# Kernel optimization log

Measured on AMD Instinct MI355X. Metric: run time of the kernel, lower is better.

The kernel has to match this reference:

```python
import jax, jax.numpy as jnp
import numpy as np

B, T, D = 2, 2048, 1024
H = 16
DH = D // H


def setup_inputs() -> dict:
    key = jax.random.key(0)
    ks = jax.random.split(key, 6)
    s = 1.0 / np.sqrt(D)
    return {
        "input_emb": jax.random.normal(ks[0], (B, T, D), dtype=jnp.float32),
        "W_key": jax.random.normal(ks[1], (D, D), dtype=jnp.float32) * s,
        "W_query": jax.random.normal(ks[2], (D, D), dtype=jnp.float32) * s,
        "W_value": jax.random.normal(ks[3], (D, D), dtype=jnp.float32) * s,
        "W_out": jax.random.normal(ks[4], (D, D), dtype=jnp.float32) * s,
        "b_out": jnp.zeros((D,), dtype=jnp.float32),
    }


def reference(input_emb, W_key, W_query, W_value, W_out, b_out):
    b, t, _ = input_emb.shape
    # projections (no bias on K/Q/V, matching bias_on=False)
    k = (input_emb @ W_key).reshape(b, t, H, DH).transpose(0, 2, 1, 3)    # [b,h,t,dh]
    q = (input_emb @ W_query).reshape(b, t, H, DH).transpose(0, 2, 1, 3)
    v = (input_emb @ W_value).reshape(b, t, H, DH).transpose(0, 2, 1, 3)
    # NOTE: source computes K @ Q^T (not Q @ K^T) — reproduce faithfully.
    scores = jnp.einsum("bhid,bhjd->bhij", k, q) / jnp.sqrt(jnp.float32(DH))
    mask = jnp.triu(jnp.ones((t, t), dtype=bool), k=1)                    # True where j > i
    scores = jnp.where(mask, -jnp.inf, scores)
    attn = jax.nn.softmax(scores, axis=-1)                                # softmax over j (query axis)
    ctx = jnp.einsum("bhij,bhjd->bhid", attn, v)                          # [b,h,t,dh]
    ctx = ctx.transpose(0, 2, 1, 3).reshape(b, t, H * DH)                 # [b,t,d]
    return ctx @ W_out + b_out
```

## Files before the change

kernel.cpp:

```cpp
#include <hip/hip_runtime.h>
#include <cstdint>
#include <cstddef>

#define T_SEQ 2048
#define DMODEL 1024
#define NHEAD 16
#define DHEAD 64
#define BATCH 2
#define MROWS (BATCH * T_SEQ)

typedef __attribute__((ext_vector_type(8))) short bf16x8;
typedef __attribute__((ext_vector_type(4))) float f32x4;
typedef unsigned int u32;

__device__ __forceinline__ unsigned short f2bf(float f) {
  u32 u = __float_as_uint(f);
  u32 r = (u + 0x7FFFu + ((u >> 16) & 1u)) >> 16;
  return (unsigned short)r;
}

__device__ __forceinline__ u32 cvtpk(float a, float b) {
  u32 r;
  asm("v_cvt_pk_bf16_f32 %0, %1, %2" : "=v"(r) : "v"(a), "v"(b));
  return r;
}

__device__ __forceinline__ void gl_lds16(const unsigned short* g, unsigned short* l) {
  __builtin_amdgcn_global_load_lds(
      (const __attribute__((address_space(1))) u32*)g,
      (__attribute__((address_space(3))) u32*)l, 16, 0, 0);
}

__global__ void k_prep(const float* __restrict__ X, unsigned short* __restrict__ Xb,
                       const float* __restrict__ W0, const float* __restrict__ W1,
                       const float* __restrict__ W2, const float* __restrict__ W3,
                       unsigned short* __restrict__ T0, unsigned short* __restrict__ T1,
                       unsigned short* __restrict__ T2, unsigned short* __restrict__ T3) {
  const int bid = blockIdx.x;
  if (bid < 4096) {
    int i = (bid * 256 + threadIdx.x) * 4;
    float4 v = *reinterpret_cast<const float4*>(X + i);
    ushort4 o;
    o.x = f2bf(v.x); o.y = f2bf(v.y); o.z = f2bf(v.z); o.w = f2bf(v.w);
    *reinterpret_cast<ushort4*>(Xb + i) = o;
    return;
  }
  const int b2 = bid - 4096;
  const int z = b2 >> 10;
  const int rem = b2 & 1023;
  const int cx = rem & 31, ry = rem >> 5;
  const float* W = (z == 0) ? W0 : (z == 1) ? W1 : (z == 2) ? W2 : W3;
  unsigned short* Wt = (z == 0) ? T0 : (z == 1) ? T1 : (z == 2) ? T2 : T3;
  __shared__ float tile[32][33];
  const int c0 = cx * 32, r0 = ry * 32;
  const int tx = threadIdx.x & 31, ty = threadIdx.x >> 5;
#pragma unroll
  for (int i = ty; i < 32; i += 8)
    tile[i][tx] = W[(size_t)(r0 + i) * DMODEL + c0 + tx];
  __syncthreads();
#pragma unroll
  for (int i = ty; i < 32; i += 8)
    Wt[(size_t)(c0 + i) * DMODEL + r0 + tx] = f2bf(tile[tx][i]);
}

__global__ __launch_bounds__(256, 2)
void k_gemm_qkv(const unsigned short* __restrict__ Xb,
                const unsigned short* __restrict__ Wkt,
                const unsigned short* __restrict__ Wqt,
                const unsigned short* __restrict__ Wvt,
                unsigned short* __restrict__ Qr,
                unsigned short* __restrict__ Kr,
                unsigned short* __restrict__ Vt)
{
  __shared__ __align__(16) unsigned short As[128 * 32];
  __shared__ __align__(16) unsigned short Bs[128 * 32];
  const int orig = blockIdx.x;
  const int t = (orig & 7) * 96 + (orig >> 3);
  const int z = t >> 8;
  const int remt = t & 255;
  const int by = remt >> 3, bx = remt & 7;
  const unsigned short* Bt = (z == 0) ? Wkt : (z == 1) ? Wqt : Wvt;

  const int tid = threadIdx.x;
  const int lane = tid & 63, w = tid >> 6;
  const int wr = w >> 1, wc = w & 1;
  const int l15 = lane & 15, l4 = lane >> 4;
  const int m0 = by * 128, n0 = bx * 128;

  f32x4 acc[4][4] = {};

  for (int k0 = 0; k0 < DMODEL; k0 += 32) {
#pragma unroll
    for (int i = 0; i < 2; ++i) {
      int c = i * 256 + tid;
      int row = c >> 2, cc = c & 3;
      gl_lds16(Xb + (size_t)(m0 + row) * DMODEL + k0 + cc * 8, As + c * 8);
      gl_lds16(Bt + (size_t)(n0 + row) * DMODEL + k0 + cc * 8, Bs + c * 8);
    }
    __syncthreads();
    bf16x8 af[4], bfr[4];
#pragma unroll
    for (int mi = 0; mi < 4; ++mi)
      af[mi] = *reinterpret_cast<const bf16x8*>(As + (wr * 64 + mi * 16 + l15) * 32 + l4 * 8);
#pragma unroll
    for (int ni = 0; ni < 4; ++ni)
      bfr[ni] = *reinterpret_cast<const bf16x8*>(Bs + (wc * 64 + ni * 16 + l15) * 32 + l4 * 8);
#pragma unroll
    for (int mi = 0; mi < 4; ++mi)
#pragma unroll
      for (int ni = 0; ni < 4; ++ni)
        acc[mi][ni] = __builtin_amdgcn_mfma_f32_16x16x32_bf16(af[mi], bfr[ni], acc[mi][ni], 0, 0, 0);
    __syncthreads();
  }

  if (z < 2) {
    unsigned short* C = (z == 0) ? Qr : Kr;
#pragma unroll
    for (int mi = 0; mi < 4; ++mi)
#pragma unroll
      for (int ni = 0; ni < 4; ++ni) {
        const int col = n0 + wc * 64 + ni * 16 + l15;
        const int rowb = m0 + wr * 64 + mi * 16 + l4 * 4;
#pragma unroll
        for (int r = 0; r < 4; ++r)
          C[(size_t)(rowb + r) * DMODEL + col] = f2bf(acc[mi][ni][r]);
      }
  } else {
#pragma unroll
    for (int mi = 0; mi < 4; ++mi)
#pragma unroll
      for (int ni = 0; ni < 4; ++ni) {
        const int col = n0 + wc * 64 + ni * 16 + l15;
        const int h = col >> 6, dh = col & 63;
        const int rowb = m0 + wr * 64 + mi * 16 + l4 * 4;
        const int b = rowb >> 11, tt = rowb & (T_SEQ - 1);
        const int tl = tt & 63;
        const int tp = (tt & ~63) | (tl & 32) | ((tl & 12) << 1) | ((tl & 16) >> 2);
        unsigned short* p = Vt + ((size_t)(b * NHEAD + h) * DHEAD + dh) * T_SEQ + tp;
        ushort4 pkv;
        pkv.x = f2bf(acc[mi][ni][0]); pkv.y = f2bf(acc[mi][ni][1]);
        pkv.z = f2bf(acc[mi][ni][2]); pkv.w = f2bf(acc[mi][ni][3]);
        *reinterpret_cast<ushort4*>(p) = pkv;
      }
  }
}

__global__ __launch_bounds__(256, 2)
void k_attn(const unsigned short* __restrict__ Qr,
            const unsigned short* __restrict__ Kr,
            const unsigned short* __restrict__ Vp,
            unsigned short* __restrict__ ctx)
{
  __shared__ __align__(16) char lds[65536];
  const int tid = threadIdx.x;
  const int lane = tid & 63, w = tid >> 6;
  const int l15 = lane & 15, l4 = lane >> 4;

  const int x = blockIdx.x;
  const int xcd = x & 7, idx = x >> 3;
  const int bh = xcd + 8 * (idx & 3);
  const int cpair = idx >> 2;
  const int b = bh >> 4, h = bh & 15;

  const unsigned short* Qbase = Qr + (size_t)b * T_SEQ * DMODEL + h * DHEAD;
  const unsigned short* Kbase = Kr + (size_t)b * T_SEQ * DMODEL + h * DHEAD;
  const unsigned short* Vbase = Vp + (size_t)bh * DHEAD * T_SEQ;
  unsigned short* obase = ctx + (size_t)b * T_SEQ * DMODEL + h * DHEAD;

  const float SC = 0.18033688011112042f;
  const float M0 = 12.0f;
  const int srow = tid >> 3, scb = tid & 7;
  const int scolE = (scb ^ (srow & 7)) << 3;

  const int sw = (l15 & 7) << 4;
  const char* aK0 = lds + l15 * 128 + ((l4 * 16) ^ sw);
  const char* aK1 = lds + l15 * 128 + (((64 + l4 * 16)) ^ sw);

  const unsigned short* kp = Kbase + (size_t)srow * DMODEL + scolE;
  const unsigned short* vpb = Vbase + (size_t)srow * T_SEQ + scolE;

#define KRD(P, st, ni, v1) (*reinterpret_cast<const bf16x8*>(((v1) ? aK1 : aK0) + (P) * 16384 + (st) * 8192 + (ni) * 2048))
#define VRD(P, st, df, hk) (*reinterpret_cast<const bf16x8*>(((hk) ? aK1 : aK0) + 32768 + (P) * 16384 + (st) * 8192 + (df) * 2048))

#define STAGE(KD, VD, kg, vg)                                                     \
      {                                                                           \
        gl_lds16((kg), (KD) + tid * 8);                                           \
        gl_lds16((kg) + 32 * DMODEL, (KD) + 2048 + tid * 8);                      \
        gl_lds16((kg) + 64 * DMODEL, (KD) + 4096 + tid * 8);                      \
        gl_lds16((kg) + 96 * DMODEL, (KD) + 6144 + tid * 8);                      \
        gl_lds16((vg), (VD) + tid * 8);                                           \
        gl_lds16((vg) + 32 * T_SEQ, (VD) + 2048 + tid * 8);                       \
        gl_lds16((vg) + 64, (VD) + 4096 + tid * 8);                               \
        gl_lds16((vg) + 32 * T_SEQ + 64, (VD) + 6144 + tid * 8);                  \
      }

#define GROUP_BODY(g, P)                                                          \
    {                                                                             \
      const int kv0 = (g) * 128;                                                  \
      const bool diag = ((g) == NG - 1);                                          \
      __builtin_amdgcn_sched_barrier(0);                                          \
      asm volatile("s_waitcnt vmcnt(0)" ::: "memory");                            \
      __builtin_amdgcn_sched_barrier(0);                                          \
      __builtin_amdgcn_s_barrier();                                               \
      __builtin_amdgcn_sched_barrier(0);                                          \
      if ((g) + 1 < NG) {                                                         \
        unsigned short* Kn = (unsigned short*)(lds + ((P) ^ 1) * 16384);          \
        unsigned short* Vn = (unsigned short*)(lds + 32768 + ((P) ^ 1) * 16384);  \
        STAGE(Kn, Vn, kstage, vstage)                                             \
        kstage += 128 * DMODEL; vstage += 128;                                    \
      }                                                                           \
      __builtin_amdgcn_sched_barrier(0);                                          \
      const bool a1 = !diag || codd;                                              \
      const int nlim0 = (diag && !codd) ? (w + 1) : 4;                            \
      const int nlim1 = (diag && codd) ? (w + 1) : 4;                             \
      f32x4 S[2][4] = {};                                                         \
      __builtin_amdgcn_s_setprio(1);                                              \
      _Pragma("unroll")                                                           \
      for (int ni = 0; ni < 4; ++ni)                                              \
        if (ni < nlim0) {                                                         \
          S[0][ni] = __builtin_amdgcn_mfma_f32_16x16x32_bf16(KRD(P, 0, ni, 0), qf[0], S[0][ni], 0, 0, 0); \
          S[0][ni] = __builtin_amdgcn_mfma_f32_16x16x32_bf16(KRD(P, 0, ni, 1), qf[1], S[0][ni], 0, 0, 0); \
        }                                                                         \
      if (a1) {                                                                   \
        _Pragma("unroll")                                                         \
        for (int ni = 0; ni < 4; ++ni)                                            \
          if (ni < nlim1) {                                                       \
            S[1][ni] = __builtin_amdgcn_mfma_f32_16x16x32_bf16(KRD(P, 1, ni, 0), qf[0], S[1][ni], 0, 0, 0); \
            S[1][ni] = __builtin_amdgcn_mfma_f32_16x16x32_bf16(KRD(P, 1, ni, 1), qf[1], S[1][ni], 0, 0, 0); \
          }                                                                       \
      }                                                                           \
      __builtin_amdgcn_s_setprio(0);                                              \
      if (diag) {                                                                 \
        if (!codd) {                                                              \
          _Pragma("unroll")                                                       \
          for (int ni = 0; ni < 4; ++ni)                                          \
            if (ni < nlim0) {                                                     \
              _Pragma("unroll")                                                   \
              for (int r = 0; r < 4; ++r)                                         \
                if (kv0 + ni * 16 + l4 * 4 + r > qrow) S[0][ni][r] = -INFINITY;   \
            }                                                                     \
        } else {                                                                  \
          _Pragma("unroll")                                                       \
          for (int ni = 0; ni < 4; ++ni)                                          \
            if (ni < nlim1) {                                                     \
              _Pragma("unroll")                                                   \
              for (int r = 0; r < 4; ++r)                                         \
                if (kv0 + 64 + ni * 16 + l4 * 4 + r > qrow) S[1][ni][r] = -INFINITY; \
            }                                                                     \
        }                                                                         \
      }                                                                           \
      union __align__(16) PW { u32 u[2][2][4]; bf16x8 v[2][2]; } pw = {};         \
      _Pragma("unroll")                                                           \
      for (int ni = 0; ni < 4; ++ni)                                              \
        if (ni < nlim0) {                                                         \
          const float p0 = __builtin_amdgcn_exp2f(__builtin_fmaf(S[0][ni][0], SC, -M0)); \
          const float p1 = __builtin_amdgcn_exp2f(__builtin_fmaf(S[0][ni][1], SC, -M0)); \
          const float p2 = __builtin_amdgcn_exp2f(__builtin_fmaf(S[0][ni][2], SC, -M0)); \
          const float p3 = __builtin_amdgcn_exp2f(__builtin_fmaf(S[0][ni][3], SC, -M0)); \
          lP += (p0 + p1) + (p2 + p3);                                            \
          pw.u[0][ni >> 1][(ni & 1) * 2]     = cvtpk(p0, p1);                     \
          pw.u[0][ni >> 1][(ni & 1) * 2 + 1] = cvtpk(p2, p3);                     \
        }                                                                         \
      if (a1) {                                                                   \
        _Pragma("unroll")                                                         \
        for (int ni = 0; ni < 4; ++ni)                                            \
          if (ni < nlim1) {                                                       \
            const float p0 = __builtin_amdgcn_exp2f(__builtin_fmaf(S[1][ni][0], SC, -M0)); \
            const float p1 = __builtin_amdgcn_exp2f(__builtin_fmaf(S[1][ni][1], SC, -M0)); \
            const float p2 = __builtin_amdgcn_exp2f(__builtin_fmaf(S[1][ni][2], SC, -M0)); \
            const float p3 = __builtin_amdgcn_exp2f(__builtin_fmaf(S[1][ni][3], SC, -M0)); \
            lP += (p0 + p1) + (p2 + p3);                                          \
            pw.u[1][ni >> 1][(ni & 1) * 2]     = cvtpk(p0, p1);                   \
            pw.u[1][ni >> 1][(ni & 1) * 2 + 1] = cvtpk(p2, p3);                   \
          }                                                                       \
      }                                                                           \
      __builtin_amdgcn_s_setprio(1);                                              \
      {                                                                           \
        const int hkl0 = (diag && !codd) ? ((nlim0 + 1) >> 1) : 2;                \
        _Pragma("unroll")                                                         \
        for (int hk = 0; hk < 2; ++hk)                                            \
          if (hk < hkl0) {                                                        \
            _Pragma("unroll")                                                     \
            for (int df = 0; df < 4; ++df)                                        \
              O[df] = __builtin_amdgcn_mfma_f32_16x16x32_bf16(VRD(P, 0, df, hk), pw.v[0][hk], O[df], 0, 0, 0); \
          }                                                                       \
      }                                                                           \
      if (a1) {                                                                   \
        const int hkl1 = (diag && codd) ? ((nlim1 + 1) >> 1) : 2;                 \
        _Pragma("unroll")                                                         \
        for (int hk = 0; hk < 2; ++hk)                                            \
          if (hk < hkl1) {                                                        \
            _Pragma("unroll")                                                     \
            for (int df = 0; df < 4; ++df)                                        \
              O[df] = __builtin_amdgcn_mfma_f32_16x16x32_bf16(VRD(P, 1, df, hk), pw.v[1][hk], O[df], 0, 0, 0); \
          }                                                                       \
      }                                                                           \
      __builtin_amdgcn_s_setprio(0);                                              \
      __builtin_amdgcn_sched_barrier(0);                                          \
    }

  for (int half = 0; half < 2; ++half) {
    const int c = half ? (31 - cpair) : cpair;
    const bool codd = (c & 1) != 0;
    const int q0w = c * 64 + w * 16;
    const int NG = (c + 2) >> 1;
    const int qrow = q0w + l15;

    bf16x8 qf[2];
#pragma unroll
    for (int ks = 0; ks < 2; ++ks)
      qf[ks] = *reinterpret_cast<const bf16x8*>(
          Qbase + (size_t)(q0w + l15) * DMODEL + ks * 32 + l4 * 8);

    __builtin_amdgcn_sched_barrier(0);
    __builtin_amdgcn_s_barrier();
    __builtin_amdgcn_sched_barrier(0);
    {
      unsigned short* Ks = (unsigned short*)(lds);
      unsigned short* Vs = (unsigned short*)(lds + 32768);
      STAGE(Ks, Vs, kp, vpb)
    }
    const unsigned short* kstage = kp + 128 * DMODEL;
    const unsigned short* vstage = vpb + 128;

    f32x4 O[4] = {};
    float lP = 0.f;

    for (int g2 = 0; g2 < NG; g2 += 2) {
      GROUP_BODY(g2, 0)
      if (g2 + 1 < NG) GROUP_BODY(g2 + 1, 1)
    }

    float lS = lP;
    lS += __shfl_xor(lS, 16);
    lS += __shfl_xor(lS, 32);
    const float rinv = 1.0f / lS;
#pragma unroll
    for (int df = 0; df < 4; ++df) {
      ushort4 o;
      o.x = f2bf(O[df][0] * rinv);
      o.y = f2bf(O[df][1] * rinv);
      o.z = f2bf(O[df][2] * rinv);
      o.w = f2bf(O[df][3] * rinv);
      *reinterpret_cast<ushort4*>(obase + (size_t)qrow * DMODEL + df * 16 + l4 * 4) = o;
    }
  }
#undef GROUP_BODY
#undef STAGE
#undef KRD
#undef VRD
}

__global__ __launch_bounds__(256, 2)
void k_gemm_out(const unsigned short* __restrict__ Ab,
                const unsigned short* __restrict__ Bt,
                const float* __restrict__ bias,
                float* __restrict__ C)
{
  __shared__ __align__(16) unsigned short As[128 * 32];
  __shared__ __align__(16) unsigned short Bs[128 * 32];
  const int orig = blockIdx.x;
  const int t = (orig & 7) * 32 + (orig >> 3);
  const int by = t >> 3, bx = t & 7;

  const int tid = threadIdx.x;
  const int lane = tid & 63, w = tid >> 6;
  const int wr = w >> 1, wc = w & 1;
  const int l15 = lane & 15, l4 = lane >> 4;
  const int m0 = by * 128, n0 = bx * 128;

  f32x4 acc[4][4] = {};

  for (int k0 = 0; k0 < DMODEL; k0 += 32) {
#pragma unroll
    for (int i = 0; i < 2; ++i) {
      int c = i * 256 + tid;
      int row = c >> 2, cc = c & 3;
      gl_lds16(Ab + (size_t)(m0 + row) * DMODEL + k0 + cc * 8, As + c * 8);
      gl_lds16(Bt + (size_t)(n0 + row) * DMODEL + k0 + cc * 8, Bs + c * 8);
    }
    __syncthreads();
    bf16x8 af[4], bfr[4];
#pragma unroll
    for (int mi = 0; mi < 4; ++mi)
      af[mi] = *reinterpret_cast<const bf16x8*>(As + (wr * 64 + mi * 16 + l15) * 32 + l4 * 8);
#pragma unroll
    for (int ni = 0; ni < 4; ++ni)
      bfr[ni] = *reinterpret_cast<const bf16x8*>(Bs + (wc * 64 + ni * 16 + l15) * 32 + l4 * 8);
#pragma unroll
    for (int mi = 0; mi < 4; ++mi)
#pragma unroll
      for (int ni = 0; ni < 4; ++ni)
        acc[mi][ni] = __builtin_amdgcn_mfma_f32_16x16x32_bf16(af[mi], bfr[ni], acc[mi][ni], 0, 0, 0);
    __syncthreads();
  }

#pragma unroll
  for (int mi = 0; mi < 4; ++mi)
#pragma unroll
    for (int ni = 0; ni < 4; ++ni) {
      const int col = n0 + wc * 64 + ni * 16 + l15;
      const float bv = bias[col];
      const int rowb = m0 + wr * 64 + mi * 16 + l4 * 4;
#pragma unroll
      for (int r = 0; r < 4; ++r)
        C[(size_t)(rowb + r) * DMODEL + col] = acc[mi][ni][r] + bv;
    }
}

extern "C" void kernel_launch(void* const* d_in, const int* in_sizes, int n_in,
                              void* d_out, int out_size, void* d_ws, size_t ws_size,
                              hipStream_t stream) {
  const float* X  = (const float*)d_in[0];
  const float* Wk = (const float*)d_in[1];
  const float* Wq = (const float*)d_in[2];
  const float* Wv = (const float*)d_in[3];
  const float* Wo = (const float*)d_in[4];
  const float* bo = (const float*)d_in[5];
  float* out = (float*)d_out;

  char* ws = (char*)d_ws;
  const size_t MB = 1024 * 1024;
  unsigned short* Xb  = (unsigned short*)(ws + 0 * MB);
  unsigned short* Wkt = (unsigned short*)(ws + 8 * MB);
  unsigned short* Wqt = (unsigned short*)(ws + 10 * MB);
  unsigned short* Wvt = (unsigned short*)(ws + 12 * MB);
  unsigned short* Wot = (unsigned short*)(ws + 14 * MB);
  unsigned short* Qr  = (unsigned short*)(ws + 16 * MB);
  unsigned short* Kr  = (unsigned short*)(ws + 24 * MB);
  unsigned short* Vt  = (unsigned short*)(ws + 32 * MB);
  unsigned short* Ctx = (unsigned short*)(ws + 40 * MB);

  k_prep<<<8192, 256, 0, stream>>>(X, Xb, Wk, Wq, Wv, Wo, Wkt, Wqt, Wvt, Wot);
  k_gemm_qkv<<<768, 256, 0, stream>>>(Xb, Wkt, Wqt, Wvt, Qr, Kr, Vt);
  k_attn<<<dim3(512), 256, 0, stream>>>(Qr, Kr, Vt, Ctx);
  k_gemm_out<<<256, 256, 0, stream>>>(Ctx, Wot, bo, out);
}
```

Measured before the change: 103.5 us.

## Double-buffer LDS tiles in QKV and output GEMMs to overlap loads with MFMA

Both projection GEMMs now use two LDS buffers per operand and prefetch the next K-slice via direct global-to-LDS loads while MFMAs run on the current slice. This replaces the load-sync-compute-sync loop with a single barrier per step. Staging addresses are precomputed, and the MFMA block is bracketed with s_setprio to favour matrix issue. LDS use per block doubles, which may limit occupancy, and the manual waitcnt and sched_barrier sequencing constrains the compiler's scheduling.

Measured after the change: 102.7 us. No clear change (-0.8%).

```diff
diff --git a/kernel.cpp b/kernel.cpp
--- a/kernel.cpp
+++ b/kernel.cpp
@@ -72,8 +72,8 @@
                 unsigned short* __restrict__ Kr,
                 unsigned short* __restrict__ Vt)
 {
-  __shared__ __align__(16) unsigned short As[128 * 32];
-  __shared__ __align__(16) unsigned short Bs[128 * 32];
+  __shared__ __align__(16) unsigned short As[2][128 * 32];
+  __shared__ __align__(16) unsigned short Bs[2][128 * 32];
   const int orig = blockIdx.x;
   const int t = (orig & 7) * 96 + (orig >> 3);
   const int z = t >> 8;
@@ -87,31 +87,59 @@
   const int l15 = lane & 15, l4 = lane >> 4;
   const int m0 = by * 128, n0 = bx * 128;
 
+  const int srow = tid >> 2, scc = tid & 3;
+  const unsigned short* Ab0 = Xb + (size_t)(m0 + srow) * DMODEL + scc * 8;
+  const unsigned short* Bb0 = Bt + (size_t)(n0 + srow) * DMODEL + scc * 8;
+  const unsigned short* Ab1 = Ab0 + (size_t)64 * DMODEL;
+  const unsigned short* Bb1 = Bb0 + (size_t)64 * DMODEL;
+
+#define GSTAGE(buf, k0)                                                   \
+  {                                                                       \
+    gl_lds16(Ab0 + (k0), As[buf] + tid * 8);                              \
+    gl_lds16(Ab1 + (k0), As[buf] + 2048 + tid * 8);                       \
+    gl_lds16(Bb0 + (k0), Bs[buf] + tid * 8);                              \
+    gl_lds16(Bb1 + (k0), Bs[buf] + 2048 + tid * 8);                       \
+  }
+
+#define GCOMP(buf)                                                        \
+  {                                                                       \
+    bf16x8 af[4], bfr[4];                                                 \
+    _Pragma("unroll")                                                     \
+    for (int mi = 0; mi < 4; ++mi)                                        \
+      af[mi] = *reinterpret_cast<const bf16x8*>(As[buf] + (wr * 64 + mi * 16 + l15) * 32 + l4 * 8); \
+    _Pragma("unroll")                                                     \
+    for (int ni = 0; ni < 4; ++ni)                                        \
+      bfr[ni] = *reinterpret_cast<const bf16x8*>(Bs[buf] + (wc * 64 + ni * 16 + l15) * 32 + l4 * 8); \
+    __builtin_amdgcn_s_setprio(1);                                        \
+    _Pragma("unroll")                                                     \
+    for (int mi = 0; mi < 4; ++mi)                                        \
+      _Pragma("unroll")                                                   \
+      for (int ni = 0; ni < 4; ++ni)                                      \
+        acc[mi][ni] = __builtin_amdgcn_mfma_f32_16x16x32_bf16(af[mi], bfr[ni], acc[mi][ni], 0, 0, 0); \
+    __builtin_amdgcn_s_setprio(0);                                        \
+  }
+
+#define GSYNC                                                             \
+  __builtin_amdgcn_sched_barrier(0);                                      \
+  asm volatile("s_waitcnt vmcnt(0)" ::: "memory");                        \
+  __builtin_amdgcn_s_barrier();                                           \
+  __builtin_amdgcn_sched_barrier(0);
+
   f32x4 acc[4][4] = {};
 
-  for (int k0 = 0; k0 < DMODEL; k0 += 32) {
-#pragma unroll
-    for (int i = 0; i < 2; ++i) {
-      int c = i * 256 + tid;
-      int row = c >> 2, cc = c & 3;
-      gl_lds16(Xb + (size_t)(m0 + row) * DMODEL + k0 + cc * 8, As + c * 8);
-      gl_lds16(Bt + (size_t)(n0 + row) * DMODEL + k0 + cc * 8, Bs + c * 8);
-    }
-    __syncthreads();
-    bf16x8 af[4], bfr[4];
-#pragma unroll
-    for (int mi = 0; mi < 4; ++mi)
-      af[mi] = *reinterpret_cast<const bf16x8*>(As + (wr * 64 + mi * 16 + l15) * 32 + l4 * 8);
-#pragma unroll
-    for (int ni = 0; ni < 4; ++ni)
-      bfr[ni] = *reinterpret_cast<const bf16x8*>(Bs + (wc * 64 + ni * 16 + l15) * 32 + l4 * 8);
-#pragma unroll
-    for (int mi = 0; mi < 4; ++mi)
-#pragma unroll
-      for (int ni = 0; ni < 4; ++ni)
-        acc[mi][ni] = __builtin_amdgcn_mfma_f32_16x16x32_bf16(af[mi], bfr[ni], acc[mi][ni], 0, 0, 0);
-    __syncthreads();
-  }
+  GSTAGE(0, 0)
+  GSYNC
+  for (int k0 = 0; k0 < DMODEL; k0 += 64) {
+    GSTAGE(1, k0 + 32)
+    GCOMP(0)
+    GSYNC
+    if (k0 + 64 < DMODEL) { GSTAGE(0, k0 + 64) }
+    GCOMP(1)
+    GSYNC
+  }
+#undef GSTAGE
+#undef GCOMP
+#undef GSYNC
 
   if (z < 2) {
     unsigned short* C = (z == 0) ? Qr : Kr;
@@ -357,8 +385,8 @@
                 const float* __restrict__ bias,
                 float* __restrict__ C)
 {
-  __shared__ __align__(16) unsigned short As[128 * 32];
-  __shared__ __align__(16) unsigned short Bs[128 * 32];
+  __shared__ __align__(16) unsigned short As[2][128 * 32];
+  __shared__ __align__(16) unsigned short Bs[2][128 * 32];
   const int orig = blockIdx.x;
   const int t = (orig & 7) * 32 + (orig >> 3);
   const int by = t >> 3, bx = t & 7;
@@ -369,31 +397,59 @@
   const int l15 = lane & 15, l4 = lane >> 4;
   const int m0 = by * 128, n0 = bx * 128;
 
+  const int srow = tid >> 2, scc = tid & 3;
+  const unsigned short* Ab0 = Ab + (size_t)(m0 + srow) * DMODEL + scc * 8;
+  const unsigned short* Bb0 = Bt + (size_t)(n0 + srow) * DMODEL + scc * 8;
+  const unsigned short* Ab1 = Ab0 + (size_t)64 * DMODEL;
+  const unsigned short* Bb1 = Bb0 + (size_t)64 * DMODEL;
+
+#define GSTAGE(buf, k0)                                                   \
+  {                                                                       \
+    gl_lds16(Ab0 + (k0), As[buf] + tid * 8);                              \
+    gl_lds16(Ab1 + (k0), As[buf] + 2048 + tid * 8);                       \
+    gl_lds16(Bb0 + (k0), Bs[buf] + tid * 8);                              \
+    gl_lds16(Bb1 + (k0), Bs[buf] + 2048 + tid * 8);                       \
+  }
+
+#define GCOMP(buf)                                                        \
+  {                                                                       \
+    bf16x8 af[4], bfr[4];                                                 \
+    _Pragma("unroll")                                                     \
+    for (int mi = 0; mi < 4; ++mi)                                        \
+      af[mi] = *reinterpret_cast<const bf16x8*>(As[buf] + (wr * 64 + mi * 16 + l15) * 32 + l4 * 8); \
+    _Pragma("unroll")                                                     \
+    for (int ni = 0; ni < 4; ++ni)                                        \
+      bfr[ni] = *reinterpret_cast<const bf16x8*>(Bs[buf] + (wc * 64 + ni * 16 + l15) * 32 + l4 * 8); \
+    __builtin_amdgcn_s_setprio(1);                                        \
+    _Pragma("unroll")                                                     \
+    for (int mi = 0; mi < 4; ++mi)                                        \
+      _Pragma("unroll")                                                   \
+      for (int ni = 0; ni < 4; ++ni)                                      \
+        acc[mi][ni] = __builtin_amdgcn_mfma_f32_16x16x32_bf16(af[mi], bfr[ni], acc[mi][ni], 0, 0, 0); \
+    __builtin_amdgcn_s_setprio(0);                                        \
+  }
+
+#define GSYNC                                                             \
+  __builtin_amdgcn_sched_barrier(0);                                      \
+  asm volatile("s_waitcnt vmcnt(0)" ::: "memory");                        \
+  __builtin_amdgcn_s_barrier();                                           \
+  __builtin_amdgcn_sched_barrier(0);
+
   f32x4 acc[4][4] = {};
 
-  for (int k0 = 0; k0 < DMODEL; k0 += 32) {
-#pragma unroll
-    for (int i = 0; i < 2; ++i) {
-      int c = i * 256 + tid;
-      int row = c >> 2, cc = c & 3;
-      gl_lds16(Ab + (size_t)(m0 + row) * DMODEL + k0 + cc * 8, As + c * 8);
-      gl_lds16(Bt + (size_t)(n0 + row) * DMODEL + k0 + cc * 8, Bs + c * 8);
-    }
-    __syncthreads();
-    bf16x8 af[4], bfr[4];
-#pragma unroll
-    for (int mi = 0; mi < 4; ++mi)
-      af[mi] = *reinterpret_cast<const bf16x8*>(As + (wr * 64 + mi * 16 + l15) * 32 + l4 * 8);
-#pragma unroll
-    for (int ni = 0; ni < 4; ++ni)
-      bfr[ni] = *reinterpret_cast<const bf16x8*>(Bs + (wc * 64 + ni * 16 + l15) * 32 + l4 * 8);
-#pragma unroll
-    for (int mi = 0; mi < 4; ++mi)
-#pragma unroll
-      for (int ni = 0; ni < 4; ++ni)
-        acc[mi][ni] = __builtin_amdgcn_mfma_f32_16x16x32_bf16(af[mi], bfr[ni], acc[mi][ni], 0, 0, 0);
-    __syncthreads();
-  }
+  GSTAGE(0, 0)
+  GSYNC
+  for (int k0 = 0; k0 < DMODEL; k0 += 64) {
+    GSTAGE(1, k0 + 32)
+    GCOMP(0)
+    GSYNC
+    if (k0 + 64 < DMODEL) { GSTAGE(0, k0 + 64) }
+    GCOMP(1)
+    GSYNC
+  }
+#undef GSTAGE
+#undef GCOMP
+#undef GSYNC
 
 #pragma unroll
   for (int mi = 0; mi < 4; ++mi)
```
